# Optimization experiments

Measured on AMD Instinct MI355X. Metric: run time of the kernel, lower is better.

## Reference

```python
import jax, jax.numpy as jnp
import numpy as np

ALPHA, BETA, LAMDA = 0.4, 2.0, 2.0
N_VIEWS, BATCH, DIM = 12, 4096, 128


def setup_inputs() -> dict:
    key = jax.random.key(0)
    k1, k2, k3, k4 = jax.random.split(key, 4)
    return {
        "SV_A": jax.random.normal(k1, (N_VIEWS, BATCH, DIM), dtype=jnp.float32),
        "SV_N": jax.random.normal(k2, (N_VIEWS, BATCH, DIM), dtype=jnp.float32),
        "MV_A": jax.random.normal(k3, (BATCH, DIM), dtype=jnp.float32),
        "MV_N": jax.random.normal(k4, (BATCH, DIM), dtype=jnp.float32),
    }


def reference(SV_A, SV_N, MV_A, MV_N):
    # expanded pairwise SQUARED distances across views, per batch element
    diff = SV_A[:, None, :, :] - SV_N[None, :, :, :]      # [nA, nN, B, D]
    d = jnp.sum(diff * diff, axis=-1)                     # [nA, nN, B]
    nA, nN, B = d.shape

    # hard-negative (confuser) mining: globally closest cross-object view pair per sample
    idx = jnp.argmin(d.reshape(nA * nN, B), axis=0)       # [B]
    conf_A = idx // nN
    conf_N = idx % nN
    b = jnp.arange(B)
    f_conf_A = SV_A[conf_A, b, :]                         # [B, D]
    f_conf_N = SV_N[conf_N, b, :]                         # [B, D]

    # inter-class distance between MV embeddings (euclidean, matches torch.cdist)
    mv_inter = jnp.sqrt(jnp.sum((MV_A - MV_N) ** 2, axis=-1))   # [B]
    # inter-class distance between confuser embeddings (squared, matches min of d)
    mc_inter = jnp.min(d, axis=(0, 1))                           # [B]
    # intra-class distances MV <-> confuser (euclidean)
    a_clstr = jnp.sqrt(jnp.sum((MV_A - f_conf_A) ** 2, axis=-1))  # [B]
    c_intra = jnp.sqrt(jnp.sum((MV_N - f_conf_N) ** 2, axis=-1))  # [B]

    loss_m_cluster = jax.nn.relu(a_clstr - ALPHA)
    loss_c_cluster = jax.nn.relu(c_intra - ALPHA)
    loss_mc_inter = jax.nn.relu(BETA - mc_inter)
    loss_mv_inter = jax.nn.relu(BETA - mv_inter)

    losses = LAMDA * (loss_mc_inter + loss_mv_inter) + loss_m_cluster + loss_c_cluster

    info_quads = [
        jnp.count_nonzero(losses),
        jnp.mean(jnp.sqrt(mc_inter)),
        0.5 * (jnp.mean(jnp.sqrt(a_clstr)) + jnp.mean(jnp.sqrt(c_intra))),
        jnp.min(jnp.sqrt(mc_inter)),
    ]
    avg_loss = jnp.mean(losses)
    return avg_loss, info_quads
```

## Files before the change

kernel.cpp:

```cpp
#include <hip/hip_runtime.h>
#include <math.h>

#define NV 12
#define BATCH 4096
#define DIM 128
#define ALPHA_C 0.4f
#define BETA_C 2.0f
#define LAMDA_C 2.0f
#define BPB 4
#define HPAD 136
#define GPAD 26

typedef short short8 __attribute__((ext_vector_type(8)));
typedef float f32x16 __attribute__((ext_vector_type(16)));

__device__ __forceinline__ unsigned short f2bf(float f) {
    unsigned int u = __float_as_uint(f);
    return (unsigned short)((u + 0x7fffu + ((u >> 16) & 1u)) >> 16);
}
__device__ __forceinline__ float bf2f(unsigned short s) {
    return __uint_as_float(((unsigned int)s) << 16);
}

__global__ __launch_bounds__(256) void perb_kernel(
    const float* __restrict__ SV_A, const float* __restrict__ SV_N,
    const float* __restrict__ MV_A, const float* __restrict__ MV_N,
    float4* __restrict__ perb)
{
    const int wave = threadIdx.x >> 6;
    const int lane = threadIdx.x & 63;
    const int b    = blockIdx.x * BPB + wave;

    __shared__ __align__(16) unsigned short Hi[BPB][24][HPAD];
    __shared__ __align__(16) unsigned short Lo[BPB][24][HPAD];
    __shared__ __align__(16) float G[BPB][24][GPAD];

    const size_t mvoff = (size_t)b * DIM + lane;
    const float ma0 = MV_A[mvoff];
    const float ma1 = MV_A[mvoff + 64];
    const float mn0 = MV_N[mvoff];
    const float mn1 = MV_N[mvoff + 64];

    {
        const int half = lane >> 5;
        const int c4   = (lane & 31) * 4;
        #pragma unroll
        for (int rr = 0; rr < NV / 2; ++rr) {
            const int i = 2 * rr + half;
            const size_t off = ((size_t)(i * BATCH + b)) * DIM + c4;
            #pragma unroll
            for (int arr = 0; arr < 2; ++arr) {
                const float4 v = *(const float4*)((arr ? SV_N : SV_A) + off);
                const unsigned short h0 = f2bf(v.x), h1 = f2bf(v.y);
                const unsigned short h2 = f2bf(v.z), h3 = f2bf(v.w);
                const unsigned short l0 = f2bf(v.x - bf2f(h0));
                const unsigned short l1 = f2bf(v.y - bf2f(h1));
                const unsigned short l2 = f2bf(v.z - bf2f(h2));
                const unsigned short l3 = f2bf(v.w - bf2f(h3));
                const int row = arr * NV + i;
                uint2 hw, lw;
                hw.x = (unsigned int)h0 | ((unsigned int)h1 << 16);
                hw.y = (unsigned int)h2 | ((unsigned int)h3 << 16);
                lw.x = (unsigned int)l0 | ((unsigned int)l1 << 16);
                lw.y = (unsigned int)l2 | ((unsigned int)l3 << 16);
                *(uint2*)&Hi[wave][row][c4] = hw;
                *(uint2*)&Lo[wave][row][c4] = lw;
            }
        }
    }

    {
        int r = lane & 31;
        if (r >= 24) r = 0;
        const int h = lane >> 5;
        const unsigned short* hbase = &Hi[wave][r][h * 8];
        const unsigned short* lbase = &Lo[wave][r][h * 8];
        f32x16 acc = {0.f, 0.f, 0.f, 0.f, 0.f, 0.f, 0.f, 0.f,
                      0.f, 0.f, 0.f, 0.f, 0.f, 0.f, 0.f, 0.f};
        #pragma unroll
        for (int kb = 0; kb < 8; ++kb) {
            const short8 hv = *(const short8*)(hbase + kb * 16);
            const short8 lv = *(const short8*)(lbase + kb * 16);
            acc = __builtin_amdgcn_mfma_f32_32x32x16_bf16(hv, hv, acc, 0, 0, 0);
            acc = __builtin_amdgcn_mfma_f32_32x32x16_bf16(hv, lv, acc, 0, 0, 0);
            acc = __builtin_amdgcn_mfma_f32_32x32x16_bf16(lv, hv, acc, 0, 0, 0);
        }
        const int col = lane & 31;
        if (col < 24) {
            #pragma unroll
            for (int rg = 0; rg < 12; ++rg) {
                const int row = (rg & 3) + 8 * (rg >> 2) + 4 * h;
                G[wave][row][col] = acc[rg];
            }
        }
    }

    float best_d = 3.4e38f;
    int   best_p = 1 << 20;
    if (lane < 36) {
        const int i2 = lane / 6;
        const int j2 = lane % 6;
        const int ia0 = 2 * i2, ia1 = 2 * i2 + 1;
        const int jn0 = 12 + 2 * j2, jn1 = jn0 + 1;
        const float2 g0 = *(const float2*)&G[wave][ia0][jn0];
        const float2 g1 = *(const float2*)&G[wave][ia1][jn0];
        const float na0 = G[wave][ia0][ia0];
        const float na1 = G[wave][ia1][ia1];
        const float nn0 = G[wave][jn0][jn0];
        const float nn1 = G[wave][jn1][jn1];
        const float d00 = na0 + nn0 - 2.f * g0.x;
        const float d01 = na0 + nn1 - 2.f * g0.y;
        const float d10 = na1 + nn0 - 2.f * g1.x;
        const float d11 = na1 + nn1 - 2.f * g1.y;
        const int p00 = ia0 * NV + 2 * j2;
        best_d = d00; best_p = p00;
        if (d01 < best_d) { best_d = d01; best_p = p00 + 1; }
        if (d10 < best_d) { best_d = d10; best_p = p00 + NV; }
        if (d11 < best_d) { best_d = d11; best_p = p00 + NV + 1; }
    }
    #pragma unroll
    for (int off = 32; off > 0; off >>= 1) {
        const float od = __shfl_down(best_d, off, 64);
        const int   op = __shfl_down(best_p, off, 64);
        if (od < best_d || (od == best_d && op < best_p)) { best_d = od; best_p = op; }
    }
    best_d = __shfl(best_d, 0, 64);
    best_p = __shfl(best_p, 0, 64);

    const int istar = best_p / NV;
    const int jstar = best_p % NV;

    float sa, sc, sm;
    {
        const size_t offA = ((size_t)(istar * BATCH + b)) * DIM + lane;
        const size_t offN = ((size_t)(jstar * BATCH + b)) * DIM + lane;
        const float fa0 = SV_A[offA];
        const float fa1 = SV_A[offA + 64];
        const float fn0 = SV_N[offN];
        const float fn1 = SV_N[offN + 64];
        float d1;
        d1 = ma0 - fa0; sa  = d1 * d1;
        d1 = ma1 - fa1; sa += d1 * d1;
        d1 = mn0 - fn0; sc  = d1 * d1;
        d1 = mn1 - fn1; sc += d1 * d1;
        d1 = ma0 - mn0; sm  = d1 * d1;
        d1 = ma1 - mn1; sm += d1 * d1;
    }
    #pragma unroll
    for (int off = 32; off > 0; off >>= 1) {
        sa += __shfl_down(sa, off, 64);
        sc += __shfl_down(sc, off, 64);
        sm += __shfl_down(sm, off, 64);
    }

    if (lane == 0) {
        const float mc    = fmaxf(best_d, 0.f);
        const float a_cl  = sqrtf(sa);
        const float c_in  = sqrtf(sc);
        const float mv_in = sqrtf(sm);
        const float loss  = LAMDA_C * (fmaxf(BETA_C - mc, 0.f) + fmaxf(BETA_C - mv_in, 0.f))
                          + fmaxf(a_cl - ALPHA_C, 0.f) + fmaxf(c_in - ALPHA_C, 0.f);
        float4 o;
        o.x = loss;
        o.y = (loss != 0.f) ? 1.f : 0.f;
        o.z = sqrtf(mc);
        o.w = 0.5f * (sqrtf(a_cl) + sqrtf(c_in));
        perb[b] = o;
    }
}

__global__ __launch_bounds__(1024) void final_kernel(
    const float4* __restrict__ perb, float* __restrict__ out)
{
    const int t = threadIdx.x;
    float sl = 0.f, sn = 0.f, ss = 0.f, sh = 0.f, mnv = 3.4e38f;
    #pragma unroll
    for (int u = 0; u < BATCH / 1024; ++u) {
        const float4 v = perb[t + u * 1024];
        sl += v.x; sn += v.y; ss += v.z; sh += v.w;
        mnv = fminf(mnv, v.z);
    }
    #pragma unroll
    for (int off = 32; off > 0; off >>= 1) {
        sl += __shfl_down(sl, off, 64);
        sn += __shfl_down(sn, off, 64);
        ss += __shfl_down(ss, off, 64);
        sh += __shfl_down(sh, off, 64);
        mnv = fminf(mnv, __shfl_down(mnv, off, 64));
    }
    __shared__ float r[16][5];
    const int w = t >> 6;
    if ((t & 63) == 0) {
        r[w][0] = sl; r[w][1] = sn; r[w][2] = ss; r[w][3] = sh; r[w][4] = mnv;
    }
    __syncthreads();
    if (t == 0) {
        #pragma unroll
        for (int i = 1; i < 16; ++i) {
            sl += r[i][0]; sn += r[i][1]; ss += r[i][2]; sh += r[i][3];
            mnv = fminf(mnv, r[i][4]);
        }
        const float inv = 1.0f / (float)BATCH;
        out[0] = sl * inv;
        out[1] = sn;
        out[2] = ss * inv;
        out[3] = sh * inv;
        out[4] = mnv;
    }
}

extern "C" void kernel_launch(void* const* d_in, const int* in_sizes, int n_in,
                              void* d_out, int out_size, void* d_ws, size_t ws_size,
                              hipStream_t stream) {
    const float* SV_A = (const float*)d_in[0];
    const float* SV_N = (const float*)d_in[1];
    const float* MV_A = (const float*)d_in[2];
    const float* MV_N = (const float*)d_in[3];
    float* out = (float*)d_out;
    float4* perb = (float4*)d_ws;

    perb_kernel<<<BATCH / BPB, 256, 0, stream>>>(SV_A, SV_N, MV_A, MV_N, perb);
    final_kernel<<<1, 1024, 0, stream>>>(perb, out);
}
```

Measured before the change: 97.65 us.

## Fuse final reduction into main kernel via last-block atomic counter

Replaces the separate single-block final reduction kernel with a last-block-done pattern. Each block reduces its four per-sample results in shared memory and writes one partial record, then bumps an atomic counter, and the last block reduces all partials and writes the outputs. The bf16 hi/lo split also switches from hand-written rounding to packed HIP bf16 conversion intrinsics. This removes one kernel launch and its dependency gap, but adds a memset launch and atomic traffic, and the result depends on the atomic ordering being correct.

New measurement: 112.4 us. 15.1% more time.

```diff
diff --git a/kernel.cpp b/kernel.cpp
--- a/kernel.cpp
+++ b/kernel.cpp
@@ -1,4 +1,5 @@
 #include <hip/hip_runtime.h>
+#include <hip/hip_bf16.h>
 #include <math.h>
 
 #define NV 12
@@ -8,24 +9,18 @@
 #define BETA_C 2.0f
 #define LAMDA_C 2.0f
 #define BPB 4
+#define NB (BATCH / BPB)
 #define HPAD 136
 #define GPAD 26
 
 typedef short short8 __attribute__((ext_vector_type(8)));
 typedef float f32x16 __attribute__((ext_vector_type(16)));
-
-__device__ __forceinline__ unsigned short f2bf(float f) {
-    unsigned int u = __float_as_uint(f);
-    return (unsigned short)((u + 0x7fffu + ((u >> 16) & 1u)) >> 16);
-}
-__device__ __forceinline__ float bf2f(unsigned short s) {
-    return __uint_as_float(((unsigned int)s) << 16);
-}
 
 __global__ __launch_bounds__(256) void perb_kernel(
     const float* __restrict__ SV_A, const float* __restrict__ SV_N,
     const float* __restrict__ MV_A, const float* __restrict__ MV_N,
-    float4* __restrict__ perb)
+    float* __restrict__ partials, unsigned int* __restrict__ counter,
+    float* __restrict__ out)
 {
     const int wave = threadIdx.x >> 6;
     const int lane = threadIdx.x & 63;
@@ -34,6 +29,8 @@
     __shared__ __align__(16) unsigned short Hi[BPB][24][HPAD];
     __shared__ __align__(16) unsigned short Lo[BPB][24][HPAD];
     __shared__ __align__(16) float G[BPB][24][GPAD];
+    __shared__ float comm[BPB][5];
+    __shared__ int   lastf;
 
     const size_t mvoff = (size_t)b * DIM + lane;
     const float ma0 = MV_A[mvoff];
@@ -51,18 +48,20 @@
             #pragma unroll
             for (int arr = 0; arr < 2; ++arr) {
                 const float4 v = *(const float4*)((arr ? SV_N : SV_A) + off);
-                const unsigned short h0 = f2bf(v.x), h1 = f2bf(v.y);
-                const unsigned short h2 = f2bf(v.z), h3 = f2bf(v.w);
-                const unsigned short l0 = f2bf(v.x - bf2f(h0));
-                const unsigned short l1 = f2bf(v.y - bf2f(h1));
-                const unsigned short l2 = f2bf(v.z - bf2f(h2));
-                const unsigned short l3 = f2bf(v.w - bf2f(h3));
+                const __hip_bfloat162 h01 = __float22bfloat162_rn({v.x, v.y});
+                const __hip_bfloat162 h23 = __float22bfloat162_rn({v.z, v.w});
+                const float lx = v.x - __bfloat162float(h01.x);
+                const float ly = v.y - __bfloat162float(h01.y);
+                const float lz = v.z - __bfloat162float(h23.x);
+                const float lw_ = v.w - __bfloat162float(h23.y);
+                const __hip_bfloat162 l01 = __float22bfloat162_rn({lx, ly});
+                const __hip_bfloat162 l23 = __float22bfloat162_rn({lz, lw_});
                 const int row = arr * NV + i;
                 uint2 hw, lw;
-                hw.x = (unsigned int)h0 | ((unsigned int)h1 << 16);
-                hw.y = (unsigned int)h2 | ((unsigned int)h3 << 16);
-                lw.x = (unsigned int)l0 | ((unsigned int)l1 << 16);
-                lw.y = (unsigned int)l2 | ((unsigned int)l3 << 16);
+                hw.x = *(const unsigned int*)&h01;
+                hw.y = *(const unsigned int*)&h23;
+                lw.x = *(const unsigned int*)&l01;
+                lw.y = *(const unsigned int*)&l23;
                 *(uint2*)&Hi[wave][row][c4] = hw;
                 *(uint2*)&Lo[wave][row][c4] = lw;
             }
@@ -160,52 +159,73 @@
         const float mv_in = sqrtf(sm);
         const float loss  = LAMDA_C * (fmaxf(BETA_C - mc, 0.f) + fmaxf(BETA_C - mv_in, 0.f))
                           + fmaxf(a_cl - ALPHA_C, 0.f) + fmaxf(c_in - ALPHA_C, 0.f);
-        float4 o;
-        o.x = loss;
-        o.y = (loss != 0.f) ? 1.f : 0.f;
-        o.z = sqrtf(mc);
-        o.w = 0.5f * (sqrtf(a_cl) + sqrtf(c_in));
-        perb[b] = o;
-    }
-}
-
-__global__ __launch_bounds__(1024) void final_kernel(
-    const float4* __restrict__ perb, float* __restrict__ out)
-{
-    const int t = threadIdx.x;
-    float sl = 0.f, sn = 0.f, ss = 0.f, sh = 0.f, mnv = 3.4e38f;
-    #pragma unroll
-    for (int u = 0; u < BATCH / 1024; ++u) {
-        const float4 v = perb[t + u * 1024];
-        sl += v.x; sn += v.y; ss += v.z; sh += v.w;
-        mnv = fminf(mnv, v.z);
-    }
-    #pragma unroll
-    for (int off = 32; off > 0; off >>= 1) {
-        sl += __shfl_down(sl, off, 64);
-        sn += __shfl_down(sn, off, 64);
-        ss += __shfl_down(ss, off, 64);
-        sh += __shfl_down(sh, off, 64);
-        mnv = fminf(mnv, __shfl_down(mnv, off, 64));
-    }
-    __shared__ float r[16][5];
-    const int w = t >> 6;
-    if ((t & 63) == 0) {
-        r[w][0] = sl; r[w][1] = sn; r[w][2] = ss; r[w][3] = sh; r[w][4] = mnv;
+        const float z = sqrtf(mc);
+        comm[wave][0] = loss;
+        comm[wave][1] = (loss != 0.f) ? 1.f : 0.f;
+        comm[wave][2] = z;
+        comm[wave][3] = 0.5f * (sqrtf(a_cl) + sqrtf(c_in));
+        comm[wave][4] = z;
     }
     __syncthreads();
-    if (t == 0) {
-        #pragma unroll
-        for (int i = 1; i < 16; ++i) {
-            sl += r[i][0]; sn += r[i][1]; ss += r[i][2]; sh += r[i][3];
-            mnv = fminf(mnv, r[i][4]);
-        }
-        const float inv = 1.0f / (float)BATCH;
-        out[0] = sl * inv;
-        out[1] = sn;
-        out[2] = ss * inv;
-        out[3] = sh * inv;
-        out[4] = mnv;
+
+    if (threadIdx.x == 0) {
+        float sl = 0.f, sn = 0.f, ss = 0.f, sh = 0.f, mn = 3.4e38f;
+        #pragma unroll
+        for (int w = 0; w < BPB; ++w) {
+            sl += comm[w][0]; sn += comm[w][1]; ss += comm[w][2]; sh += comm[w][3];
+            mn = fminf(mn, comm[w][4]);
+        }
+        float* rec = partials + (size_t)blockIdx.x * 8;
+        __hip_atomic_store(&rec[0], sl, __ATOMIC_RELAXED, __HIP_MEMORY_SCOPE_AGENT);
+        __hip_atomic_store(&rec[1], sn, __ATOMIC_RELAXED, __HIP_MEMORY_SCOPE_AGENT);
+        __hip_atomic_store(&rec[2], ss, __ATOMIC_RELAXED, __HIP_MEMORY_SCOPE_AGENT);
+        __hip_atomic_store(&rec[3], sh, __ATOMIC_RELAXED, __HIP_MEMORY_SCOPE_AGENT);
+        __hip_atomic_store(&rec[4], mn, __ATOMIC_RELAXED, __HIP_MEMORY_SCOPE_AGENT);
+        const unsigned int old =
+            __hip_atomic_fetch_add(counter, 1u, __ATOMIC_ACQ_REL, __HIP_MEMORY_SCOPE_AGENT);
+        lastf = (old == NB - 1) ? 1 : 0;
+    }
+    __syncthreads();
+
+    if (lastf) {
+        const int t = threadIdx.x;
+        float sl = 0.f, sn = 0.f, ss = 0.f, sh = 0.f, mn = 3.4e38f;
+        #pragma unroll
+        for (int u = 0; u < NB / 256; ++u) {
+            const float* rec = partials + (size_t)(t + u * 256) * 8;
+            sl += __hip_atomic_load(&rec[0], __ATOMIC_RELAXED, __HIP_MEMORY_SCOPE_AGENT);
+            sn += __hip_atomic_load(&rec[1], __ATOMIC_RELAXED, __HIP_MEMORY_SCOPE_AGENT);
+            ss += __hip_atomic_load(&rec[2], __ATOMIC_RELAXED, __HIP_MEMORY_SCOPE_AGENT);
+            sh += __hip_atomic_load(&rec[3], __ATOMIC_RELAXED, __HIP_MEMORY_SCOPE_AGENT);
+            mn = fminf(mn,
+                 __hip_atomic_load(&rec[4], __ATOMIC_RELAXED, __HIP_MEMORY_SCOPE_AGENT));
+        }
+        #pragma unroll
+        for (int off = 32; off > 0; off >>= 1) {
+            sl += __shfl_down(sl, off, 64);
+            sn += __shfl_down(sn, off, 64);
+            ss += __shfl_down(ss, off, 64);
+            sh += __shfl_down(sh, off, 64);
+            mn = fminf(mn, __shfl_down(mn, off, 64));
+        }
+        if ((t & 63) == 0) {
+            comm[t >> 6][0] = sl; comm[t >> 6][1] = sn; comm[t >> 6][2] = ss;
+            comm[t >> 6][3] = sh; comm[t >> 6][4] = mn;
+        }
+        __syncthreads();
+        if (t == 0) {
+            #pragma unroll
+            for (int w = 1; w < BPB; ++w) {
+                sl += comm[w][0]; sn += comm[w][1]; ss += comm[w][2]; sh += comm[w][3];
+                mn = fminf(mn, comm[w][4]);
+            }
+            const float inv = 1.0f / (float)BATCH;
+            out[0] = sl * inv;
+            out[1] = sn;
+            out[2] = ss * inv;
+            out[3] = sh * inv;
+            out[4] = mn;
+        }
     }
 }
 
@@ -217,8 +237,10 @@
     const float* MV_A = (const float*)d_in[2];
     const float* MV_N = (const float*)d_in[3];
     float* out = (float*)d_out;
-    float4* perb = (float4*)d_ws;
-
-    perb_kernel<<<BATCH / BPB, 256, 0, stream>>>(SV_A, SV_N, MV_A, MV_N, perb);
-    final_kernel<<<1, 1024, 0, stream>>>(perb, out);
+
+    float* partials = (float*)d_ws;
+    unsigned int* counter = (unsigned int*)((char*)d_ws + NB * 8 * sizeof(float));
+
+    hipMemsetAsync(counter, 0, sizeof(unsigned int), stream);
+    perb_kernel<<<NB, 256, 0, stream>>>(SV_A, SV_N, MV_A, MV_N, partials, counter, out);
 }
```
